# Optimization experiments

Hardware: AMD Instinct MI355X
Metric: run time of the kernel (lower is better)

Reference implementation:

```python
import jax, jax.numpy as jnp
import numpy as np

B, C, H, W = 4, 3, 256, 256
L, WIDTH, M1, M2 = 4, 32, 12, 12


def setup_inputs() -> dict:
    key = jax.random.key(0)
    ks = jax.random.split(key, 13)
    scale = 1.0 / (WIDTH * WIDTH)
    return {
        "x": jax.random.uniform(ks[0], (B, C, H, W), jnp.float32),
        "p_w": jax.random.normal(ks[1], (C + 2, WIDTH), jnp.float32) * 0.3,
        "p_b": jax.random.normal(ks[2], (WIDTH,), jnp.float32) * 0.1,
        "sw1r": scale * jax.random.uniform(ks[3], (L, WIDTH, WIDTH, M1, M2), jnp.float32),
        "sw1i": scale * jax.random.uniform(ks[4], (L, WIDTH, WIDTH, M1, M2), jnp.float32),
        "sw2r": scale * jax.random.uniform(ks[5], (L, WIDTH, WIDTH, M1, M2), jnp.float32),
        "sw2i": scale * jax.random.uniform(ks[6], (L, WIDTH, WIDTH, M1, M2), jnp.float32),
        "cw": jax.random.normal(ks[7], (L, WIDTH, WIDTH), jnp.float32) * 0.15,
        "cb": jax.random.normal(ks[8], (L, WIDTH), jnp.float32) * 0.1,
        "mlp0_w": jax.random.normal(ks[9], (WIDTH, 128), jnp.float32) * 0.15,
        "mlp0_b": jax.random.normal(ks[10], (128,), jnp.float32) * 0.1,
        "mlp1_w": jax.random.normal(ks[11], (128, C), jnp.float32) * 0.1,
        "mlp1_b": jax.random.normal(ks[12], (C,), jnp.float32) * 0.1,
    }


def _spectral_conv(h, w1, w2):
    # h: (B, Cin, H, W); w1/w2: (Cin, Cout, M1, M2) complex
    b, ci, hh, ww = h.shape
    hf = jnp.fft.rfft2(h)  # (B, Cin, H, W//2+1)
    out_ft = jnp.zeros((b, w1.shape[1], hf.shape[2], hf.shape[3]), jnp.complex64)
    out_ft = out_ft.at[:, :, :M1, :M2].set(
        jnp.einsum('bixy,ioxy->boxy', hf[:, :, :M1, :M2], w1))
    out_ft = out_ft.at[:, :, -M1:, :M2].set(
        jnp.einsum('bixy,ioxy->boxy', hf[:, :, -M1:, :M2], w2))
    return jnp.fft.irfft2(out_ft, s=(hh, ww))


def reference(x, p_w, p_b, sw1r, sw1i, sw2r, sw2i, cw, cb, mlp0_w, mlp0_b, mlp1_w, mlp1_b):
    b, c, hh, ww = x.shape
    gx = jnp.broadcast_to(jnp.linspace(0.0, 1.0, hh)[None, :, None, None], (b, hh, ww, 1))
    gy = jnp.broadcast_to(jnp.linspace(0.0, 1.0, ww)[None, None, :, None], (b, hh, ww, 1))
    feat = jnp.concatenate([x.transpose(0, 2, 3, 1), gx, gy], axis=-1)  # (B,H,W,C+2)
    h = (feat @ p_w + p_b).transpose(0, 3, 1, 2)  # (B, width, H, W)
    for l in range(L):
        w1 = sw1r[l] + 1j * sw1i[l]
        w2 = sw2r[l] + 1j * sw2i[l]
        bypass = jnp.einsum('bihw,io->bohw', h, cw[l]) + cb[l][None, :, None, None]
        h2 = _spectral_conv(h, w1, w2) + bypass
        h = jax.nn.gelu(h2, approximate=False) if l < L - 1 else h2
    h = h.transpose(0, 2, 3, 1)  # (B,H,W,width)
    h = jax.nn.gelu(h @ mlp0_w + mlp0_b, approximate=False)
    out = h @ mlp1_w + mlp1_b
    return out.transpose(0, 3, 1, 2)  # (B, out_channels, H, W)
```

## Files before the change

kernel.cpp:

```cpp
#include <hip/hip_runtime.h>
#include <math.h>


#define ANG0 0.024543692606170260f

typedef __attribute__((ext_vector_type(8))) short bf16x8_t;
typedef __attribute__((ext_vector_type(4))) float f32x4_t;

__device__ __forceinline__ float fgelu(float v) {
    float u = v * 0.70710678118f;
    float a = fabsf(u);
    float t = __builtin_amdgcn_rcpf(__builtin_fmaf(0.3275911f, a, 1.0f));
    float p = t * __builtin_fmaf(t, __builtin_fmaf(t, __builtin_fmaf(t,
                  __builtin_fmaf(t, 1.061405429f, -1.453152027f),
                  1.421413741f), -0.284496736f), 0.254829592f);
    float e = __expf(-u * u);
    float er = __builtin_fmaf(-p, e, 1.0f);
    er = copysignf(er, u);
    return 0.5f * v * (1.0f + er);
}

__device__ __forceinline__ unsigned packsplit(float v) {
    unsigned u = __float_as_uint(v);
    unsigned hi = u & 0xffff0000u;
    float r = v - __uint_as_float(hi);
    return hi | (__float_as_uint(r) >> 16);
}

__device__ __forceinline__ void fill_csp(float2* sCSP, int tid, int nthr) {
    for (int p = tid; p < 256; p += nthr)
        sCSP[p] = make_float2(cosf(p * ANG0), sinf(p * ANG0));
}

__device__ __forceinline__ void ky_dft_tail(const float* sVp, const float2* sCSP,
                                            float* tmp, int b, int x, int y) {
    for (int idx = y; idx < 384; idx += 256) {
        int o = idx / 12, ky = idx % 12;
        const float* vp = sVp + o * 258;
        float vdc = vp[0], v128 = vp[256];
        float aR0 = vdc + ((ky & 1) ? -v128 : v128);
        float aR1 = 0.f, aI0 = 0.f, aI1 = 0.f;
#pragma unroll 4
        for (int yy = 1; yy <= 126; yy += 2) {
            int p0 = (ky * yy) & 255;
            int p1 = (p0 + ky) & 255;
            float2 c0 = sCSP[p0], c1 = sCSP[p1];
            float2 v0 = *reinterpret_cast<const float2*>(vp + 2 * yy);
            float2 v1 = *reinterpret_cast<const float2*>(vp + 2 * (yy + 1));
            aR0 = __builtin_fmaf(v0.x + v0.y, c0.x, aR0);
            aI0 = __builtin_fmaf(v0.x - v0.y, -c0.y, aI0);
            aR1 = __builtin_fmaf(v1.x + v1.y, c1.x, aR1);
            aI1 = __builtin_fmaf(v1.x - v1.y, -c1.y, aI1);
        }
        {
            int p = (ky * 127) & 255;
            float2 c = sCSP[p];
            float2 v0 = *reinterpret_cast<const float2*>(vp + 254);
            aR0 = __builtin_fmaf(v0.x + v0.y, c.x, aR0);
            aI0 = __builtin_fmaf(v0.x - v0.y, -c.y, aI0);
        }
        reinterpret_cast<float2*>(tmp + (((size_t)(b * 32 + o)) * 256 + x) * 24)[ky] =
            make_float2(aR0 + aR1, aI0 + aI1);
    }
}

__device__ __forceinline__ float c2val(int y, int j) {
    if (j >= 24 || j == 1) return 0.f;
    if (j == 0) return 1.f;
    int q = j >> 1;
    float ang = ((q * y) & 255) * ANG0;
    return (j & 1) ? -2.f * sinf(ang) : 2.f * cosf(ang);
}
__device__ __forceinline__ float etval(int j, int y) {
    if (j >= 24) return 0.f;
    int q = j >> 1;
    float ang = ((q * y) & 255) * ANG0;
    return (j & 1) ? -sinf(ang) : cosf(ang);
}
__device__ __forceinline__ void pack2(unsigned* dsthi, unsigned* dstlo,
                                      float v0, float v1) {
    unsigned u0 = __float_as_uint(v0), u1 = __float_as_uint(v1);
    *dsthi = ((u1 >> 16) << 16) | (u0 >> 16);
    float r0 = v0 - __uint_as_float(u0 & 0xffff0000u);
    float r1 = v1 - __uint_as_float(u1 & 0xffff0000u);
    *dstlo = ((__float_as_uint(r1) >> 16) << 16) | (__float_as_uint(r0) >> 16);
}

__global__ void k_init(const float* __restrict__ w0, const float* __restrict__ b0,
                       const float* __restrict__ w1, const float* __restrict__ cw,
                       unsigned* __restrict__ specA, unsigned* __restrict__ tailA,
                       unsigned* __restrict__ cwB, unsigned* __restrict__ wB,
                       float* __restrict__ w1p) {
    int t = threadIdx.x;
    const float SC = 1.0f / 65536.0f;
    for (int idx = t; idx < 4096; idx += 256) {
        int w = idx & 3, lane = (idx >> 2) & 63, mt = idx >> 8;
        int y = mt * 16 + (lane & 15);
        int j0 = 8 * (lane >> 4) + 2 * w;
        pack2(&specA[idx], &specA[4096 + idx],
              c2val(y, j0) * SC, c2val(y, j0 + 1) * SC);
    }
    for (int idx = t; idx < 4096; idx += 256) {
        int w = idx & 3, lane = (idx >> 2) & 63, tt = idx >> 8;
        int kk = tt >> 1, mtj = tt & 1;
        int j = mtj * 16 + (lane & 15);
        int y0 = kk * 32 + 8 * (lane >> 4) + 2 * w;
        pack2(&tailA[idx], &tailA[4096 + idx], etval(j, y0), etval(j, y0 + 1));
    }
    for (int idx = t; idx < 2048; idx += 256) {
        int w = idx & 3, lane = (idx >> 2) & 63, tt = idx >> 8;
        int l = tt >> 1, n = tt & 1;
        int o = n * 16 + (lane & 15);
        int i0 = 8 * (lane >> 4) + 2 * w;
        pack2(&cwB[idx], &cwB[2048 + idx],
              cw[l * 1024 + i0 * 32 + o], cw[l * 1024 + (i0 + 1) * 32 + o]);
    }
    for (int idx = t; idx < 2048; idx += 256) {
        int jw = idx & 3, lane = (idx >> 2) & 63, n = idx >> 8;
        int i0 = 8 * (lane >> 4) + 2 * jw;
        int km = n * 16 + (lane & 15);
        pack2(&wB[idx], &wB[2048 + idx], w0[i0 * 128 + km], w0[(i0 + 1) * 128 + km]);
    }
    for (int idx = t; idx < 384; idx += 256) {
        int c = idx >> 7, km = idx & 127;
        w1p[idx] = w1[km * 3 + c];
    }
}

__global__ __launch_bounds__(256, 4) void k_liftf(const float* __restrict__ xin,
                                                  const float* __restrict__ pw,
                                                  const float* __restrict__ pb,
                                                  unsigned* __restrict__ h,
                                                  float* __restrict__ tmp) {
    __shared__ float sVp[32 * 258];
    __shared__ float2 sCSP[256];
    int b = blockIdx.x >> 8, x = blockIdx.x & 255, y = threadIdx.x;
    fill_csp(sCSP, y, 256);
    int vslot = 2 * ((y <= 128) ? y : 256 - y) + ((y > 128) ? 1 : 0);
    float f0 = xin[((b * 3 + 0) * 256 + x) * 256 + y];
    float f1 = xin[((b * 3 + 1) * 256 + x) * 256 + y];
    float f2 = xin[((b * 3 + 2) * 256 + x) * 256 + y];
    float gx = x * (1.0f / 255.0f), gy = y * (1.0f / 255.0f);
#pragma unroll
    for (int o = 0; o < 32; ++o) {
        float v = pb[o] + f0 * pw[o] + f1 * pw[32 + o] + f2 * pw[64 + o]
                + gx * pw[96 + o] + gy * pw[128 + o];
        h[((b * 32 + o) * 256 + x) * 256 + y] = packsplit(v);
        sVp[o * 258 + vslot] = v;
    }
    __syncthreads();
    ky_dft_tail(sVp, sCSP, tmp, b, x, y);
}

__global__ __launch_bounds__(320) void k_dftx(const float* __restrict__ tmp,
                                              float* __restrict__ hfp) {
    __shared__ float sT[1536];
    __shared__ float2 sCSP[256];
    int plane = blockIdx.x >> 2, part = blockIdx.x & 3;
    int x0 = part * 64;
    int tid = threadIdx.x;
    fill_csp(sCSP, tid, 320);
    for (int idx = tid; idx < 1536; idx += 320)
        sT[idx] = tmp[(size_t)plane * 6144 + x0 * 24 + idx];
    __syncthreads();
    if (tid < 288) {
        int kxi = tid / 12, ky = tid % 12;
        int kxv = kxi < 12 ? kxi : 232 + kxi;
        float aR = 0.f, aI = 0.f;
        for (int xp = 0; xp < 64; ++xp) {
            int p = (kxv * (x0 + xp)) & 255;
            float2 cs2 = sCSP[p];
            float tr = sT[xp * 24 + 2 * ky], ti = sT[xp * 24 + 2 * ky + 1];
            aR += tr * cs2.x + ti * cs2.y;
            aI += ti * cs2.x - tr * cs2.y;
        }
        hfp[(((size_t)part * 128 + plane) * 24 + kxi) * 24 + 2 * ky]     = aR;
        hfp[(((size_t)part * 128 + plane) * 24 + kxi) * 24 + 2 * ky + 1] = aI;
    }
}

__global__ __launch_bounds__(320) void k_mixcinv(const float* __restrict__ hfp,
                                                 const float* __restrict__ w1r,
                                                 const float* __restrict__ w1i,
                                                 const float* __restrict__ w2r,
                                                 const float* __restrict__ w2i,
                                                 float* __restrict__ g, int l) {
    __shared__ float sA[576];
    __shared__ float2 sCSP[256];
    int b = blockIdx.x >> 5, o = blockIdx.x & 31;
    int tid = threadIdx.x;
    fill_csp(sCSP, tid, 320);
    if (tid < 288) {
        int kxi = tid / 12, ky = tid % 12;
        const float *wr, *wi;
        int rk;
        if (kxi < 12) { wr = w1r; wi = w1i; rk = kxi; }
        else          { wr = w2r; wi = w2i; rk = kxi - 12; }
        size_t wbase = ((size_t)l * 32 * 32) * 144 + (size_t)o * 144 + rk * 12 + ky;
        size_t hbase = (((size_t)(b * 32)) * 24 + kxi) * 24 + 2 * ky;
        float aR = 0.f, aI = 0.f;
#pragma unroll 4
        for (int i = 0; i < 32; ++i) {
            float2 h0 = *reinterpret_cast<const float2*>(hfp + hbase + i * 576);
            float2 h1 = *reinterpret_cast<const float2*>(hfp + 73728 + hbase + i * 576);
            float2 h2 = *reinterpret_cast<const float2*>(hfp + 147456 + hbase + i * 576);
            float2 h3 = *reinterpret_cast<const float2*>(hfp + 221184 + hbase + i * 576);
            float hr = h0.x + h1.x + h2.x + h3.x;
            float hi = h0.y + h1.y + h2.y + h3.y;
            float wrv = wr[wbase + (size_t)i * 4608];
            float wiv = wi[wbase + (size_t)i * 4608];
            aR += hr * wrv - hi * wiv;
            aI += hr * wiv + hi * wrv;
        }
        sA[kxi * 24 + 2 * ky]     = aR;
        sA[kxi * 24 + 2 * ky + 1] = aI;
    }
    __syncthreads();
    if (tid < 256) {
        int x = tid;
        float out[24];
#pragma unroll
        for (int j = 0; j < 24; ++j) out[j] = 0.f;
        for (int kxi = 0; kxi < 24; ++kxi) {
            int kxv = kxi < 12 ? kxi : 232 + kxi;
            int p = (kxv * x) & 255;
            float2 cs2 = sCSP[p];
#pragma unroll
            for (int ky = 0; ky < 12; ++ky) {
                float ar = sA[kxi * 24 + 2 * ky], ai = sA[kxi * 24 + 2 * ky + 1];
                out[2 * ky]     += ar * cs2.x - ai * cs2.y;
                out[2 * ky + 1] += ar * cs2.y + ai * cs2.x;
            }
        }
        float* gp = g + ((size_t)(b * 32 + o)) * 6144 + x * 24;
#pragma unroll
        for (int j = 0; j < 24; ++j) gp[j] = out[j];
    }
}

template <int ACT, int WRITEH>
__device__ __forceinline__ void dinv_phaseA(const unsigned* __restrict__ hU,
                                            unsigned* __restrict__ hW,
                                            const float* __restrict__ g,
                                            const unsigned* __restrict__ specA,
                                            const unsigned* __restrict__ cwB,
                                            const float* __restrict__ cb,
                                            unsigned* sVvT, int b, int x, int l,
                                            int wv, int lane) {
    int l15 = lane & 15, l4 = lane >> 4;
    unsigned hbuf[4][8];
    {
        const unsigned* hp = hU + (size_t)(b * 32) * 65536 + x * 256;
#pragma unroll
        for (int mtl = 0; mtl < 4; ++mtl) {
            int mtg = wv * 4 + mtl;
#pragma unroll
            for (int j = 0; j < 8; ++j)
                hbuf[mtl][j] = hp[(size_t)(8 * l4 + j) * 65536 + mtg * 16 + l15];
        }
    }
    bf16x8_t Ghi[2], Glo[2];
#pragma unroll
    for (int n = 0; n < 2; ++n) {
        float gv[8];
        if (l4 < 3) {
            const float* gp = g + (size_t)(b * 32 + n * 16 + l15) * 6144
                            + x * 24 + 8 * l4;
            float4 a = *reinterpret_cast<const float4*>(gp);
            float4 c = *reinterpret_cast<const float4*>(gp + 4);
            gv[0] = a.x; gv[1] = a.y; gv[2] = a.z; gv[3] = a.w;
            gv[4] = c.x; gv[5] = c.y; gv[6] = c.z; gv[7] = c.w;
        } else {
#pragma unroll
            for (int j = 0; j < 8; ++j) gv[j] = 0.f;
        }
#pragma unroll
        for (int j = 0; j < 8; ++j) {
            float v = gv[j];
            unsigned u = __float_as_uint(v);
            Ghi[n][j] = (short)(u >> 16);
            float r = v - __uint_as_float(u & 0xffff0000u);
            Glo[n][j] = (short)(__float_as_uint(r) >> 16);
        }
    }
    bf16x8_t Whi[2], Wlo[2];
#pragma unroll
    for (int n = 0; n < 2; ++n) {
        Whi[n] = *reinterpret_cast<const bf16x8_t*>(cwB + ((l * 2 + n) * 64 + lane) * 4);
        Wlo[n] = *reinterpret_cast<const bf16x8_t*>(cwB + 2048 + ((l * 2 + n) * 64 + lane) * 4);
    }
    float cbb[2] = {cb[l * 32 + l15], cb[l * 32 + 16 + l15]};
#pragma unroll
    for (int mtl = 0; mtl < 4; ++mtl) {
        int mtg = wv * 4 + mtl;
        bf16x8_t C2hi = *reinterpret_cast<const bf16x8_t*>(specA + (mtg * 64 + lane) * 4);
        bf16x8_t C2lo = *reinterpret_cast<const bf16x8_t*>(specA + 4096 + (mtg * 64 + lane) * 4);
        bf16x8_t Hhi, Hlo;
#pragma unroll
        for (int j = 0; j < 8; ++j) {
            unsigned u = hbuf[mtl][j];
            Hhi[j] = (short)(u >> 16);
            Hlo[j] = (short)(u & 0xffffu);
        }
#pragma unroll
        for (int n = 0; n < 2; ++n) {
            f32x4_t acc = {0.f, 0.f, 0.f, 0.f};
            acc = __builtin_amdgcn_mfma_f32_16x16x32_bf16(C2hi, Ghi[n], acc, 0, 0, 0);
            acc = __builtin_amdgcn_mfma_f32_16x16x32_bf16(C2lo, Ghi[n], acc, 0, 0, 0);
            acc = __builtin_amdgcn_mfma_f32_16x16x32_bf16(C2hi, Glo[n], acc, 0, 0, 0);
            acc = __builtin_amdgcn_mfma_f32_16x16x32_bf16(Hhi, Whi[n], acc, 0, 0, 0);
            acc = __builtin_amdgcn_mfma_f32_16x16x32_bf16(Hlo, Whi[n], acc, 0, 0, 0);
            acc = __builtin_amdgcn_mfma_f32_16x16x32_bf16(Hhi, Wlo[n], acc, 0, 0, 0);
            uint4 pu;
            {
                float v0 = acc[0] + cbb[n], v1 = acc[1] + cbb[n];
                float v2 = acc[2] + cbb[n], v3 = acc[3] + cbb[n];
                if (ACT) { v0 = fgelu(v0); v1 = fgelu(v1); v2 = fgelu(v2); v3 = fgelu(v3); }
                pu.x = packsplit(v0); pu.y = packsplit(v1);
                pu.z = packsplit(v2); pu.w = packsplit(v3);
            }
            *reinterpret_cast<uint4*>(&sVvT[(n * 16 + l15) * 260 + mtg * 16 + l4 * 4]) = pu;
            if (WRITEH)
                *reinterpret_cast<uint4*>(hW + (size_t)(b * 32 + n * 16 + l15) * 65536
                                          + x * 256 + mtg * 16 + l4 * 4) = pu;
        }
    }
}

__global__ __launch_bounds__(256) void k_dinvf(unsigned* __restrict__ h,
                                               const float* __restrict__ g,
                                               const unsigned* __restrict__ specA,
                                               const unsigned* __restrict__ tailA,
                                               const unsigned* __restrict__ cwB,
                                               const float* __restrict__ cb,
                                               float* __restrict__ tmp, int l) {
    __shared__ unsigned sVvT[32 * 260];
    int b = blockIdx.x >> 8, x = blockIdx.x & 255;
    int tid = threadIdx.x, wv = tid >> 6, lane = tid & 63;
    int l15 = lane & 15, l4 = lane >> 4;
    dinv_phaseA<1, 1>(h, h, g, specA, cwB, cb, sVvT, b, x, l, wv, lane);
    __syncthreads();
    {
        int mtj = wv >> 1, nq = wv & 1;
        f32x4_t acc = {0.f, 0.f, 0.f, 0.f};
        for (int kk = 0; kk < 8; ++kk) {
            bf16x8_t Ehi = *reinterpret_cast<const bf16x8_t*>(
                tailA + ((kk * 2 + mtj) * 64 + lane) * 4);
            bf16x8_t Elo = *reinterpret_cast<const bf16x8_t*>(
                tailA + 4096 + ((kk * 2 + mtj) * 64 + lane) * 4);
            int base = (nq * 16 + l15) * 260 + kk * 32 + 8 * l4;
            uint4 va = *reinterpret_cast<const uint4*>(&sVvT[base]);
            uint4 vb = *reinterpret_cast<const uint4*>(&sVvT[base + 4]);
            bf16x8_t Vhi, Vlo;
            Vhi[0] = (short)(va.x >> 16); Vlo[0] = (short)(va.x & 0xffffu);
            Vhi[1] = (short)(va.y >> 16); Vlo[1] = (short)(va.y & 0xffffu);
            Vhi[2] = (short)(va.z >> 16); Vlo[2] = (short)(va.z & 0xffffu);
            Vhi[3] = (short)(va.w >> 16); Vlo[3] = (short)(va.w & 0xffffu);
            Vhi[4] = (short)(vb.x >> 16); Vlo[4] = (short)(vb.x & 0xffffu);
            Vhi[5] = (short)(vb.y >> 16); Vlo[5] = (short)(vb.y & 0xffffu);
            Vhi[6] = (short)(vb.z >> 16); Vlo[6] = (short)(vb.z & 0xffffu);
            Vhi[7] = (short)(vb.w >> 16); Vlo[7] = (short)(vb.w & 0xffffu);
            acc = __builtin_amdgcn_mfma_f32_16x16x32_bf16(Ehi, Vhi, acc, 0, 0, 0);
            acc = __builtin_amdgcn_mfma_f32_16x16x32_bf16(Ehi, Vlo, acc, 0, 0, 0);
            acc = __builtin_amdgcn_mfma_f32_16x16x32_bf16(Elo, Vhi, acc, 0, 0, 0);
        }
        int j0 = mtj * 16 + l4 * 4;
        if (j0 < 24) {
            float4 st = {acc[0], acc[1], acc[2], acc[3]};
            *reinterpret_cast<float4*>(
                tmp + (size_t)(b * 32 + nq * 16 + l15) * 6144 + x * 24 + j0) = st;
        }
    }
}

__global__ __launch_bounds__(256) void k_dinvmlp(const unsigned* __restrict__ h,
                                                 const float* __restrict__ g,
                                                 const unsigned* __restrict__ specA,
                                                 const unsigned* __restrict__ cwB,
                                                 const float* __restrict__ cb,
                                                 const unsigned* __restrict__ wB,
                                                 const float* __restrict__ b0,
                                                 const float* __restrict__ w1p,
                                                 const float* __restrict__ b1,
                                                 float* __restrict__ out) {
    __shared__ unsigned sVvT[32 * 260];
    __shared__ float sOut[256 * 5];
    int b = blockIdx.x >> 8, x = blockIdx.x & 255;
    int tid = threadIdx.x, wv = tid >> 6, lane = tid & 63;
    int l15 = lane & 15, l4 = lane >> 4;
    dinv_phaseA<0, 0>(h, nullptr, g, specA, cwB, cb, sVvT, b, x, 3, wv, lane);
    __syncthreads();
    bf16x8_t Ahi[4], Alo[4];
#pragma unroll
    for (int mt = 0; mt < 4; ++mt) {
        int rowY = (wv << 6) + (mt << 4) + l15;
#pragma unroll
        for (int j = 0; j < 8; ++j) {
            unsigned u = sVvT[(8 * l4 + j) * 260 + rowY];
            Ahi[mt][j] = (short)(u >> 16);
            Alo[mt][j] = (short)(u & 0xffffu);
        }
    }
    float apart[4][4][3];
#pragma unroll
    for (int mt = 0; mt < 4; ++mt)
#pragma unroll
        for (int r = 0; r < 4; ++r)
#pragma unroll
            for (int c = 0; c < 3; ++c) apart[mt][r][c] = 0.f;
    for (int n = 0; n < 8; ++n) {
        bf16x8_t Bhi = *reinterpret_cast<const bf16x8_t*>(wB + (n * 64 + lane) * 4);
        bf16x8_t Blo = *reinterpret_cast<const bf16x8_t*>(wB + 2048 + (n * 64 + lane) * 4);
        int km = (n << 4) + l15;
        float b0v  = b0[km];
        float w1v0 = w1p[km], w1v1 = w1p[128 + km], w1v2 = w1p[256 + km];
#pragma unroll
        for (int mt = 0; mt < 4; ++mt) {
            f32x4_t acc = {0.f, 0.f, 0.f, 0.f};
            acc = __builtin_amdgcn_mfma_f32_16x16x32_bf16(Ahi[mt], Bhi, acc, 0, 0, 0);
            acc = __builtin_amdgcn_mfma_f32_16x16x32_bf16(Ahi[mt], Blo, acc, 0, 0, 0);
            acc = __builtin_amdgcn_mfma_f32_16x16x32_bf16(Alo[mt], Bhi, acc, 0, 0, 0);
#pragma unroll
            for (int r = 0; r < 4; ++r) {
                float tg = fgelu(acc[r] + b0v);
                apart[mt][r][0] = __builtin_fmaf(tg, w1v0, apart[mt][r][0]);
                apart[mt][r][1] = __builtin_fmaf(tg, w1v1, apart[mt][r][1]);
                apart[mt][r][2] = __builtin_fmaf(tg, w1v2, apart[mt][r][2]);
            }
        }
    }
#pragma unroll
    for (int mt = 0; mt < 4; ++mt)
#pragma unroll
        for (int r = 0; r < 4; ++r)
#pragma unroll
            for (int c = 0; c < 3; ++c) {
                float v = apart[mt][r][c];
                v += __shfl_xor(v, 1);
                v += __shfl_xor(v, 2);
                v += __shfl_xor(v, 4);
                v += __shfl_xor(v, 8);
                if (l15 == 0)
                    sOut[((wv << 6) + (mt << 4) + (l4 << 2) + r) * 5 + c] = v;
            }
    __syncthreads();
    float b1v0 = b1[0], b1v1 = b1[1], b1v2 = b1[2];
    out[(((size_t)b * 3 + 0) * 256 + x) * 256 + tid] = sOut[tid * 5 + 0] + b1v0;
    out[(((size_t)b * 3 + 1) * 256 + x) * 256 + tid] = sOut[tid * 5 + 1] + b1v1;
    out[(((size_t)b * 3 + 2) * 256 + x) * 256 + tid] = sOut[tid * 5 + 2] + b1v2;
}

extern "C" void kernel_launch(void* const* d_in, const int* in_sizes, int n_in,
                              void* d_out, int out_size, void* d_ws, size_t ws_size,
                              hipStream_t stream) {
    const float* xin  = (const float*)d_in[0];
    const float* pw   = (const float*)d_in[1];
    const float* pb   = (const float*)d_in[2];
    const float* sw1r = (const float*)d_in[3];
    const float* sw1i = (const float*)d_in[4];
    const float* sw2r = (const float*)d_in[5];
    const float* sw2i = (const float*)d_in[6];
    const float* cw   = (const float*)d_in[7];
    const float* cb   = (const float*)d_in[8];
    const float* w0   = (const float*)d_in[9];
    const float* b0   = (const float*)d_in[10];
    const float* w1   = (const float*)d_in[11];
    const float* b1   = (const float*)d_in[12];
    float* out = (float*)d_out;

    unsigned* specA = (unsigned*)d_ws;
    unsigned* tailA = specA + 8192;
    unsigned* cwB   = tailA + 8192;
    unsigned* wB    = cwB + 4096;
    float* w1p = (float*)(wB + 4096);
    unsigned* h = (unsigned*)(w1p + 384);
    float* tmp = (float*)(h + 8388608);
    float* hfp = tmp + 786432;
    float* g   = tmp;

    k_init<<<1, 256, 0, stream>>>(w0, b0, w1, cw, specA, tailA, cwB, wB, w1p);
    k_liftf<<<1024, 256, 0, stream>>>(xin, pw, pb, h, tmp);
    for (int l = 0; l < 4; ++l) {
        k_dftx<<<512, 320, 0, stream>>>(tmp, hfp);
        k_mixcinv<<<128, 320, 0, stream>>>(hfp, sw1r, sw1i, sw2r, sw2i, g, l);
        if (l < 3)
            k_dinvf<<<1024, 256, 0, stream>>>(h, g, specA, tailA, cwB, cb, tmp, l);
        else
            k_dinvmlp<<<1024, 256, 0, stream>>>(h, g, specA, cwB, cb, wB, b0, w1p,
                                                b1, out);
    }
}
```

Baseline: 218.5 us.

## Store hidden activations channel-last so per-pixel channel loads vectorize

Changes the packed hidden-state buffer from channel-planar (B,C,H,W) to pixel-major (B,H,W,C). The lift kernel now writes 32 channels per pixel as uint4 stores, and the inverse-DFT phase reads 8 consecutive channels per lane as two uint4 loads instead of eight strided scalar loads. The h writeback in dinv_phaseA becomes four scalar stores strided by 32 words. This trades a wide read pattern for scattered writes, and any other consumer of h not shown here must agree with the new layout.

```diff
diff --git a/kernel.cpp b/kernel.cpp
--- a/kernel.cpp
+++ b/kernel.cpp
@@ -141,12 +141,17 @@
     float f1 = xin[((b * 3 + 1) * 256 + x) * 256 + y];
     float f2 = xin[((b * 3 + 2) * 256 + x) * 256 + y];
     float gx = x * (1.0f / 255.0f), gy = y * (1.0f / 255.0f);
+    unsigned* hp = h + ((size_t)blockIdx.x * 256 + y) * 32;
+    unsigned hw[4];
 #pragma unroll
     for (int o = 0; o < 32; ++o) {
         float v = pb[o] + f0 * pw[o] + f1 * pw[32 + o] + f2 * pw[64 + o]
                 + gx * pw[96 + o] + gy * pw[128 + o];
-        h[((b * 32 + o) * 256 + x) * 256 + y] = packsplit(v);
+        hw[o & 3] = packsplit(v);
         sVp[o * 258 + vslot] = v;
+        if ((o & 3) == 3)
+            *reinterpret_cast<uint4*>(hp + (o - 3)) =
+                make_uint4(hw[0], hw[1], hw[2], hw[3]);
     }
     __syncthreads();
     ky_dft_tail(sVp, sCSP, tmp, b, x, y);
@@ -248,16 +253,16 @@
                                             unsigned* sVvT, int b, int x, int l,
                                             int wv, int lane) {
     int l15 = lane & 15, l4 = lane >> 4;
+    size_t pixbase = ((size_t)(b * 256 + x)) * 8192;
     unsigned hbuf[4][8];
-    {
-        const unsigned* hp = hU + (size_t)(b * 32) * 65536 + x * 256;
-#pragma unroll
-        for (int mtl = 0; mtl < 4; ++mtl) {
-            int mtg = wv * 4 + mtl;
-#pragma unroll
-            for (int j = 0; j < 8; ++j)
-                hbuf[mtl][j] = hp[(size_t)(8 * l4 + j) * 65536 + mtg * 16 + l15];
-        }
+#pragma unroll
+    for (int mtl = 0; mtl < 4; ++mtl) {
+        int y0 = (wv * 4 + mtl) * 16 + l15;
+        const uint4* p = reinterpret_cast<const uint4*>(
+            hU + pixbase + (size_t)y0 * 32 + 8 * l4);
+        uint4 a = p[0], c = p[1];
+        hbuf[mtl][0] = a.x; hbuf[mtl][1] = a.y; hbuf[mtl][2] = a.z; hbuf[mtl][3] = a.w;
+        hbuf[mtl][4] = c.x; hbuf[mtl][5] = c.y; hbuf[mtl][6] = c.z; hbuf[mtl][7] = c.w;
     }
     bf16x8_t Ghi[2], Glo[2];
 #pragma unroll
@@ -311,18 +316,22 @@
             acc = __builtin_amdgcn_mfma_f32_16x16x32_bf16(Hhi, Whi[n], acc, 0, 0, 0);
             acc = __builtin_amdgcn_mfma_f32_16x16x32_bf16(Hlo, Whi[n], acc, 0, 0, 0);
             acc = __builtin_amdgcn_mfma_f32_16x16x32_bf16(Hhi, Wlo[n], acc, 0, 0, 0);
-            uint4 pu;
+            unsigned puv[4];
             {
                 float v0 = acc[0] + cbb[n], v1 = acc[1] + cbb[n];
                 float v2 = acc[2] + cbb[n], v3 = acc[3] + cbb[n];
                 if (ACT) { v0 = fgelu(v0); v1 = fgelu(v1); v2 = fgelu(v2); v3 = fgelu(v3); }
-                pu.x = packsplit(v0); pu.y = packsplit(v1);
-                pu.z = packsplit(v2); pu.w = packsplit(v3);
+                puv[0] = packsplit(v0); puv[1] = packsplit(v1);
+                puv[2] = packsplit(v2); puv[3] = packsplit(v3);
             }
-            *reinterpret_cast<uint4*>(&sVvT[(n * 16 + l15) * 260 + mtg * 16 + l4 * 4]) = pu;
-            if (WRITEH)
-                *reinterpret_cast<uint4*>(hW + (size_t)(b * 32 + n * 16 + l15) * 65536
-                                          + x * 256 + mtg * 16 + l4 * 4) = pu;
+            *reinterpret_cast<uint4*>(&sVvT[(n * 16 + l15) * 260 + mtg * 16 + l4 * 4]) =
+                make_uint4(puv[0], puv[1], puv[2], puv[3]);
+            if (WRITEH) {
+#pragma unroll
+                for (int r = 0; r < 4; ++r)
+                    hW[pixbase + (size_t)(mtg * 16 + l4 * 4 + r) * 32
+                       + n * 16 + l15] = puv[r];
+            }
         }
     }
 }
```

Result: no change. 222.8 us (+1.9%).
